# Performance work log

Measured on AMD Instinct MI355X. Metric: run time of the kernel, lower is better.

## Reference

```python
import jax, jax.numpy as jnp
import numpy as np

N_NODES = 100000
N_EDGES = 1600000
IN_C, HID_C, OUT_C = 128, 128, 64


def gcn_conv(x, src, dst, n_nodes, W, b):
    # PyG GCNConv (normalize=True, add_self_loops=True):
    # out = D^{-1/2} (A+I) D^{-1/2} (x @ W^T) + b
    h = x @ W.T                                   # [N, out]
    deg = jax.ops.segment_sum(jnp.ones(src.shape, x.dtype), dst,
                              num_segments=n_nodes)  # includes self-loops
    dinv = jnp.where(deg > 0, jax.lax.rsqrt(deg), 0.0)
    norm = dinv[src] * dinv[dst]                  # [E+N]
    msg = h[src] * norm[:, None]                  # gather + scale
    out = jax.ops.segment_sum(msg, dst, num_segments=n_nodes)
    return out + b


def setup_inputs() -> dict:
    key = jax.random.key(0)
    ks = jax.random.split(key, 8)
    x = jax.random.normal(ks[0], (N_NODES, IN_C), dtype=jnp.float32)
    edge_index = jax.random.randint(ks[1], (2, N_EDGES), 0, N_NODES, dtype=jnp.int64)

    def lin(k, fan_out, fan_in):
        s = 1.0 / np.sqrt(fan_in)
        kw, kb = jax.random.split(k)
        W = jax.random.uniform(kw, (fan_out, fan_in), jnp.float32, -s, s)
        b = jax.random.uniform(kb, (fan_out,), jnp.float32, -s, s)
        return W, b

    W1, b1 = lin(ks[2], HID_C, IN_C)
    W2, b2 = lin(ks[3], HID_C, HID_C)
    W3, b3 = lin(ks[4], OUT_C, HID_C)
    return {"x": x, "edge_index": edge_index,
            "W1": W1, "b1": b1, "W2": W2, "b2": b2, "W3": W3, "b3": b3}


def reference(x, edge_index, W1, b1, W2, b2, W3, b3):
    n = x.shape[0]
    loop = jnp.arange(n, dtype=edge_index.dtype)
    src = jnp.concatenate([edge_index[0], loop])  # add self-loops once; identical per layer
    dst = jnp.concatenate([edge_index[1], loop])
    h = gcn_conv(x, src, dst, n, W1, b1)
    h = jax.nn.relu(h)
    h = gcn_conv(h, src, dst, n, W2, b2)
    h = jax.nn.relu(h)
    h = gcn_conv(h, src, dst, n, W3, b3)
    return h
```

## Files before the change

### kernel.cpp

```cpp
#include <hip/hip_runtime.h>


#define NPB 256
#define CAP 4672
#define BIN_WGS 512

typedef short bfrag __attribute__((ext_vector_type(8)));
typedef float f32x4 __attribute__((ext_vector_type(4)));
typedef unsigned short u16x8 __attribute__((ext_vector_type(8)));

__global__ __launch_bounds__(256) void bin_edges(const int* __restrict__ src,
                                                 const int* __restrict__ dst,
                                                 int* __restrict__ cur,
                                                 int* __restrict__ binned,
                                                 int E, int B) {
  __shared__ int lc[512];
  __shared__ int lbase[512];
  const int t = threadIdx.x;
  const int chunk = (E + BIN_WGS - 1) / BIN_WGS;
  const int e0 = blockIdx.x * chunk;
  const int e1 = min(E, e0 + chunk);

  for (int i = t; i < B; i += 256) lc[i] = 0;
  __syncthreads();
  for (int e = e0 + t; e < e1; e += 256) {
    int d = dst[e];
    atomicAdd(&lc[d >> 8], 1);
  }
  __syncthreads();
  for (int i = t; i < B; i += 256) {
    int c = lc[i];
    lbase[i] = c ? atomicAdd(&cur[i], c) : 0;
    lc[i] = 0;
  }
  __syncthreads();
  for (int e = e0 + t; e < e1; e += 256) {
    int d = dst[e];
    int s = __builtin_nontemporal_load(&src[e]);
    int bk = d >> 8;
    int p = lbase[bk] + atomicAdd(&lc[bk], 1);
    if (p < (bk + 1) * CAP)
      binned[p] = ((d & 255) << 24) | s;
  }
}

__global__ __launch_bounds__(256) void build_buckets(const int* __restrict__ binned,
                                                     const int* __restrict__ cur,
                                                     int* __restrict__ cols,
                                                     int2* __restrict__ off2,
                                                     float* __restrict__ dinv,
                                                     int N) {
  __shared__ int eb[CAP];
  __shared__ int ob[CAP];
  __shared__ int lc[256];
  __shared__ int sc[256];
  const int b = blockIdx.x;
  const int t = threadIdx.x;
  const int base = b * CAP;
  const int cntb = min(cur[b] - base, CAP);

  for (int i = t; i < cntb; i += 256) eb[i] = binned[base + i];
  lc[t] = 0;
  __syncthreads();
  for (int i = t; i < cntb; i += 256)
    atomicAdd(&lc[(unsigned)eb[i] >> 24], 1);
  __syncthreads();
  int myc = lc[t];
  sc[t] = myc;
  __syncthreads();
  for (int d = 1; d < 256; d <<= 1) {
    int a = (t >= d) ? sc[t - d] : 0;
    __syncthreads();
    sc[t] += a;
    __syncthreads();
  }
  int excl = sc[t] - myc;
  int node = b * NPB + t;
  if (node < N) {
    off2[node] = make_int2(base + excl, base + excl + myc);
    dinv[node] = rsqrtf((float)(myc + 1));
  }
  lc[t] = excl;
  __syncthreads();
  for (int i = t; i < cntb; i += 256) {
    int e = eb[i];
    int p = atomicAdd(&lc[(unsigned)e >> 24], 1);
    ob[p] = e & 0xFFFFFF;
  }
  __syncthreads();
  for (int i = t; i < cntb; i += 256) cols[base + i] = ob[i];
}

__device__ inline unsigned short bf16rne(float x) {
  unsigned u = __float_as_uint(x);
  return (unsigned short)((u + 0x7FFFu + ((u >> 16) & 1u)) >> 16);
}
__device__ inline float bf16lo(unsigned q) { return __uint_as_float(q << 16); }
__device__ inline float bf16hi(unsigned q) { return __uint_as_float(q & 0xFFFF0000u); }

__global__ __launch_bounds__(256) void split_w3(const float* __restrict__ W1,
                                                const float* __restrict__ W2,
                                                const float* __restrict__ W3,
                                                unsigned short* __restrict__ w1h,
                                                unsigned short* __restrict__ w1l,
                                                unsigned short* __restrict__ w2h,
                                                unsigned short* __restrict__ w2l,
                                                unsigned short* __restrict__ w3h,
                                                unsigned short* __restrict__ w3l,
                                                int* __restrict__ cur, int B) {
  int i = blockIdx.x * 256 + threadIdx.x;
  const float* W;
  unsigned short *hi, *lo;
  int j;
  if (i < 16384) {
    W = W1; hi = w1h; lo = w1l; j = i;
  } else if (i < 32768) {
    W = W2; hi = w2h; lo = w2l; j = i - 16384;
  } else if (i < 40960) {
    W = W3; hi = w3h; lo = w3l; j = i - 32768;
  } else if (i < 40960 + B) {
    cur[i - 40960] = (i - 40960) * CAP;
    return;
  } else {
    return;
  }
  float v = W[j];
  unsigned short h = bf16rne(v);
  hi[j] = h;
  lo[j] = bf16rne(v - __uint_as_float((unsigned)h << 16));
}

#define LDP 136

template <int OUTC, bool CSOUT>
__global__ __launch_bounds__(256) void gemm_planes(const unsigned short* __restrict__ Xh,
                                                   const unsigned short* __restrict__ Xl,
                                                   const unsigned short* __restrict__ Whg,
                                                   const unsigned short* __restrict__ Wlg,
                                                   const float* __restrict__ dinv,
                                                   unsigned short* __restrict__ Y,
                                                   int M) {
  constexpr int CHUNKS = OUTC / 64;
  __shared__ unsigned short Whi[64 * LDP], Wlo[64 * LDP];
  const int tid = threadIdx.x;
  const int m_base = blockIdx.x * 64;
  const int lane = tid & 63;
  const int wv = tid >> 6;
  const int col_l = lane & 15;
  const int quad = lane >> 4;
  const size_t arow = (size_t)min(m_base + wv * 16 + col_l, M - 1) * 128;
  const int bBase = col_l * LDP + quad * 8;

  bfrag aH[4], aL[4];
#pragma unroll
  for (int ks = 0; ks < 4; ++ks) {
    aH[ks] = *(const bfrag*)(Xh + arow + ks * 32 + quad * 8);
    aL[ks] = *(const bfrag*)(Xl + arow + ks * 32 + quad * 8);
  }

  f32x4 acc[CHUNKS][4];
#pragma unroll
  for (int c2 = 0; c2 < CHUNKS; ++c2)
#pragma unroll
    for (int t = 0; t < 4; ++t) acc[c2][t] = {0.f, 0.f, 0.f, 0.f};

#pragma unroll
  for (int c2 = 0; c2 < CHUNKS; ++c2) {
    if (c2) __syncthreads();
    for (int idx = tid; idx < 64 * 16; idx += 256) {
      int r = idx >> 4, g = idx & 15;
      *(u16x8*)(Whi + r * LDP + g * 8) =
          *(const u16x8*)(Whg + (size_t)(c2 * 64 + r) * 128 + g * 8);
      *(u16x8*)(Wlo + r * LDP + g * 8) =
          *(const u16x8*)(Wlg + (size_t)(c2 * 64 + r) * 128 + g * 8);
    }
    __syncthreads();
#pragma unroll
    for (int ks = 0; ks < 4; ++ks) {
#pragma unroll
      for (int t = 0; t < 4; ++t) {
        int bo = bBase + t * 16 * LDP + ks * 32;
        bfrag bHi = *(const bfrag*)(Whi + bo);
        bfrag bLo = *(const bfrag*)(Wlo + bo);
        acc[c2][t] = __builtin_amdgcn_mfma_f32_16x16x32_bf16(aH[ks], bHi, acc[c2][t], 0, 0, 0);
        acc[c2][t] = __builtin_amdgcn_mfma_f32_16x16x32_bf16(aL[ks], bHi, acc[c2][t], 0, 0, 0);
        acc[c2][t] = __builtin_amdgcn_mfma_f32_16x16x32_bf16(aH[ks], bLo, acc[c2][t], 0, 0, 0);
      }
    }
  }

#pragma unroll
  for (int r = 0; r < 4; ++r) {
    int row = m_base + wv * 16 + quad * 4 + r;
    if (row < M) {
      float s = dinv[row];
#pragma unroll
      for (int c2 = 0; c2 < CHUNKS; ++c2)
#pragma unroll
        for (int t = 0; t < 4; ++t) {
          unsigned short h = bf16rne(acc[c2][t][r] * s);
          if (CSOUT)
            Y[((size_t)c2 * M + row) * 64 + t * 16 + col_l] = h;
          else
            Y[(size_t)row * OUTC + c2 * 64 + t * 16 + col_l] = h;
        }
    }
  }
}

template <int OUTC, bool CSOUT>
__global__ __launch_bounds__(256) void gemm_xsplit(const float* __restrict__ X,
                                                   const unsigned short* __restrict__ Whg,
                                                   const unsigned short* __restrict__ Wlg,
                                                   const float* __restrict__ dinv,
                                                   unsigned short* __restrict__ Y,
                                                   int M) {
  constexpr int CHUNKS = OUTC / 64;
  __shared__ unsigned short Whi[64 * LDP], Wlo[64 * LDP];
  const int tid = threadIdx.x;
  const int m_base = blockIdx.x * 64;
  const int lane = tid & 63;
  const int wv = tid >> 6;
  const int col_l = lane & 15;
  const int quad = lane >> 4;
  const size_t arow = (size_t)min(m_base + wv * 16 + col_l, M - 1) * 128;
  const int bBase = col_l * LDP + quad * 8;

  bfrag aH[4], aL[4];
#pragma unroll
  for (int ks = 0; ks < 4; ++ks) {
    float4 v0 = *(const float4*)(X + arow + ks * 32 + quad * 8);
    float4 v1 = *(const float4*)(X + arow + ks * 32 + quad * 8 + 4);
    float vv[8] = {v0.x, v0.y, v0.z, v0.w, v1.x, v1.y, v1.z, v1.w};
#pragma unroll
    for (int j = 0; j < 8; ++j) {
      unsigned short h = bf16rne(vv[j]);
      aH[ks][j] = (short)h;
      aL[ks][j] = (short)bf16rne(vv[j] - __uint_as_float((unsigned)h << 16));
    }
  }

  f32x4 acc[CHUNKS][4];
#pragma unroll
  for (int c2 = 0; c2 < CHUNKS; ++c2)
#pragma unroll
    for (int t = 0; t < 4; ++t) acc[c2][t] = {0.f, 0.f, 0.f, 0.f};

#pragma unroll
  for (int c2 = 0; c2 < CHUNKS; ++c2) {
    if (c2) __syncthreads();
    for (int idx = tid; idx < 64 * 16; idx += 256) {
      int r = idx >> 4, g = idx & 15;
      *(u16x8*)(Whi + r * LDP + g * 8) =
          *(const u16x8*)(Whg + (size_t)(c2 * 64 + r) * 128 + g * 8);
      *(u16x8*)(Wlo + r * LDP + g * 8) =
          *(const u16x8*)(Wlg + (size_t)(c2 * 64 + r) * 128 + g * 8);
    }
    __syncthreads();
#pragma unroll
    for (int ks = 0; ks < 4; ++ks) {
#pragma unroll
      for (int t = 0; t < 4; ++t) {
        int bo = bBase + t * 16 * LDP + ks * 32;
        bfrag bHi = *(const bfrag*)(Whi + bo);
        bfrag bLo = *(const bfrag*)(Wlo + bo);
        acc[c2][t] = __builtin_amdgcn_mfma_f32_16x16x32_bf16(aH[ks], bHi, acc[c2][t], 0, 0, 0);
        acc[c2][t] = __builtin_amdgcn_mfma_f32_16x16x32_bf16(aL[ks], bHi, acc[c2][t], 0, 0, 0);
        acc[c2][t] = __builtin_amdgcn_mfma_f32_16x16x32_bf16(aH[ks], bLo, acc[c2][t], 0, 0, 0);
      }
    }
  }

#pragma unroll
  for (int r = 0; r < 4; ++r) {
    int row = m_base + wv * 16 + quad * 4 + r;
    if (row < M) {
      float s = dinv[row];
#pragma unroll
      for (int c2 = 0; c2 < CHUNKS; ++c2)
#pragma unroll
        for (int t = 0; t < 4; ++t) {
          unsigned short h = bf16rne(acc[c2][t][r] * s);
          if (CSOUT)
            Y[((size_t)c2 * M + row) * 64 + t * 16 + col_l] = h;
          else
            Y[(size_t)row * OUTC + c2 * 64 + t * 16 + col_l] = h;
        }
    }
  }
}

__device__ inline void acc_add(float* a, uint4 d) {
  a[0] += bf16lo(d.x); a[1] += bf16hi(d.x);
  a[2] += bf16lo(d.y); a[3] += bf16hi(d.y);
  a[4] += bf16lo(d.z); a[5] += bf16hi(d.z);
  a[6] += bf16lo(d.w); a[7] += bf16hi(d.w);
}

__global__ __launch_bounds__(256) void aggregate_h2(const unsigned short* __restrict__ xs,
                                                    const int2* __restrict__ off2,
                                                    const int* __restrict__ cols,
                                                    const float* __restrict__ dinv,
                                                    const float* __restrict__ bias,
                                                    unsigned short* __restrict__ oh,
                                                    unsigned short* __restrict__ ol,
                                                    int N) {
  const int cg = blockIdx.x & 1;
  const int tile = blockIdx.x >> 1;
  const int t = threadIdx.x;
  const int gl = t & 7;
  const int node = tile * 32 + (t >> 3);
  if (node >= N) return;

  const char* xb = (const char*)xs + (size_t)cg * N * 128;
  const unsigned go = (unsigned)gl * 16;

  float acc[8];
  {
    uint4 d = *(const uint4*)(xb + (size_t)node * 128 + go);
    acc[0] = bf16lo(d.x); acc[1] = bf16hi(d.x);
    acc[2] = bf16lo(d.y); acc[3] = bf16hi(d.y);
    acc[4] = bf16lo(d.z); acc[5] = bf16hi(d.z);
    acc[6] = bf16lo(d.w); acc[7] = bf16hi(d.w);
  }

  const int2 oo = off2[node];
  const int en = oo.y;
  for (int e0 = oo.x; e0 < en; e0 += 8) {
    int col = __builtin_nontemporal_load(&cols[min(e0 + gl, en - 1)]);
    int m = en - e0;
    if (m > 8) m = 8;
    const int c1 = m - 1;
    for (int j = 0; j < m; j += 4) {
      int s0 = __shfl(col, min(j,     c1), 8);
      int s1 = __shfl(col, min(j + 1, c1), 8);
      int s2 = __shfl(col, min(j + 2, c1), 8);
      int s3 = __shfl(col, min(j + 3, c1), 8);
      uint4 d0 = *(const uint4*)(xb + (size_t)s0 * 128 + go);
      uint4 d1 = *(const uint4*)(xb + (size_t)s1 * 128 + go);
      uint4 d2 = *(const uint4*)(xb + (size_t)s2 * 128 + go);
      uint4 d3 = *(const uint4*)(xb + (size_t)s3 * 128 + go);
// ... 107 lines not shown
    f32x4 oB = {h[4], h[5], h[6], h[7]};
    __builtin_nontemporal_store(oA, (f32x4*)(outf + (size_t)node * C + gl * 8));
    __builtin_nontemporal_store(oB, (f32x4*)(outf + (size_t)node * C + gl * 8 + 4));
  }
}


extern "C" void kernel_launch(void* const* d_in, const int* in_sizes, int n_in,
                              void* d_out, int out_size, void* d_ws, size_t ws_size,
                              hipStream_t stream) {
  const float* x  = (const float*)d_in[0];
  const int*   ei = (const int*)d_in[1];
  const float* W1 = (const float*)d_in[2];
  const float* b1 = (const float*)d_in[3];
  const float* W2 = (const float*)d_in[4];
  const float* b2 = (const float*)d_in[5];
  const float* W3 = (const float*)d_in[6];
  const float* b3 = (const float*)d_in[7];

  const int N = in_sizes[0] / 128;
  const int E = in_sizes[1] / 2;
  const int* src = ei;
  const int* dst = ei + E;
  const int B = (N + NPB - 1) / NPB;

  char* w = (char*)d_ws;
  size_t p = 0;
  auto alloc = [&](size_t bytes) -> void* {
    void* r = w + p;
    p = (p + bytes + 255) & ~(size_t)255;
    return r;
  };
  float*    dinv   = (float*)alloc((size_t)N * 4);
  int2*     off2   = (int2*)alloc((size_t)N * 8);
  int*      cur    = (int*)alloc((size_t)B * 4);
  int*      binned = (int*)alloc((size_t)B * CAP * 4);
  int*      cols   = (int*)alloc((size_t)B * CAP * 4);
  unsigned short* xsb = (unsigned short*)alloc((size_t)N * 128 * 2);
  unsigned short* hh  = (unsigned short*)alloc((size_t)N * 128 * 2);
  unsigned short* hl  = (unsigned short*)alloc((size_t)N * 128 * 2);
  unsigned short* w1h = (unsigned short*)alloc(128 * 128 * 2);
  unsigned short* w1l = (unsigned short*)alloc(128 * 128 * 2);
  unsigned short* w2h = (unsigned short*)alloc(128 * 128 * 2);
  unsigned short* w2l = (unsigned short*)alloc(128 * 128 * 2);
  unsigned short* w3h = (unsigned short*)alloc(64 * 128 * 2);
  unsigned short* w3l = (unsigned short*)alloc(64 * 128 * 2);

  split_w3<<<(40960 + B + 255) / 256, 256, 0, stream>>>(W1, W2, W3, w1h, w1l,
                                                        w2h, w2l, w3h, w3l,
                                                        cur, B);
  bin_edges<<<BIN_WGS, 256, 0, stream>>>(src, dst, cur, binned, E, B);
  build_buckets<<<B, 256, 0, stream>>>(binned, cur, cols, off2, dinv, N);

  const int gb = (N + 63) / 64;
  const int ah2 = ((N + 31) / 32) * 2;
  const int ab64 = (N + 31) / 32;

  gemm_xsplit<128, true><<<gb, 256, 0, stream>>>(x, w1h, w1l, dinv, xsb, N);
  aggregate_h2<<<ah2, 256, 0, stream>>>(xsb, off2, cols, dinv, b1, hh, hl, N);
  gemm_planes<128, true><<<gb, 256, 0, stream>>>(hh, hl, w2h, w2l, dinv, xsb, N);
  aggregate_h2<<<ah2, 256, 0, stream>>>(xsb, off2, cols, dinv, b2, hh, hl, N);
  gemm_planes<64, false><<<gb, 256, 0, stream>>>(hh, hl, w3h, w3l, dinv, xsb, N);
  aggregate4<64, false, false><<<ab64, 256, 0, stream>>>(xsb, off2, cols, dinv, b3,
                                                         (float*)d_out, nullptr,
                                                         nullptr, N);
}
```

Baseline: 376.2 us.

## Double GEMM row tile to 128 and split aggregation launches into halves

```diff
diff --git a/kernel.cpp b/kernel.cpp
--- a/kernel.cpp
+++ b/kernel.cpp
@@ -143,26 +143,31 @@
   constexpr int CHUNKS = OUTC / 64;
   __shared__ unsigned short Whi[64 * LDP], Wlo[64 * LDP];
   const int tid = threadIdx.x;
-  const int m_base = blockIdx.x * 64;
+  const int m_base = blockIdx.x * 128;
   const int lane = tid & 63;
   const int wv = tid >> 6;
   const int col_l = lane & 15;
   const int quad = lane >> 4;
-  const size_t arow = (size_t)min(m_base + wv * 16 + col_l, M - 1) * 128;
   const int bBase = col_l * LDP + quad * 8;
 
-  bfrag aH[4], aL[4];
-#pragma unroll
-  for (int ks = 0; ks < 4; ++ks) {
-    aH[ks] = *(const bfrag*)(Xh + arow + ks * 32 + quad * 8);
-    aL[ks] = *(const bfrag*)(Xl + arow + ks * 32 + quad * 8);
-  }
-
-  f32x4 acc[CHUNKS][4];
-#pragma unroll
-  for (int c2 = 0; c2 < CHUNKS; ++c2)
-#pragma unroll
-    for (int t = 0; t < 4; ++t) acc[c2][t] = {0.f, 0.f, 0.f, 0.f};
+  bfrag aH[2][4], aL[2][4];
+#pragma unroll
+  for (int mt = 0; mt < 2; ++mt) {
+    const size_t arow = (size_t)min(m_base + mt * 64 + wv * 16 + col_l, M - 1) * 128;
+#pragma unroll
+    for (int ks = 0; ks < 4; ++ks) {
+      aH[mt][ks] = *(const bfrag*)(Xh + arow + ks * 32 + quad * 8);
+      aL[mt][ks] = *(const bfrag*)(Xl + arow + ks * 32 + quad * 8);
+    }
+  }
+
+  f32x4 acc[2][CHUNKS][4];
+#pragma unroll
+  for (int mt = 0; mt < 2; ++mt)
+#pragma unroll
+    for (int c2 = 0; c2 < CHUNKS; ++c2)
+#pragma unroll
+      for (int t = 0; t < 4; ++t) acc[mt][c2][t] = {0.f, 0.f, 0.f, 0.f};
 
 #pragma unroll
   for (int c2 = 0; c2 < CHUNKS; ++c2) {
@@ -182,30 +187,35 @@
         int bo = bBase + t * 16 * LDP + ks * 32;
         bfrag bHi = *(const bfrag*)(Whi + bo);
         bfrag bLo = *(const bfrag*)(Wlo + bo);
-        acc[c2][t] = __builtin_amdgcn_mfma_f32_16x16x32_bf16(aH[ks], bHi, acc[c2][t], 0, 0, 0);
-        acc[c2][t] = __builtin_amdgcn_mfma_f32_16x16x32_bf16(aL[ks], bHi, acc[c2][t], 0, 0, 0);
-        acc[c2][t] = __builtin_amdgcn_mfma_f32_16x16x32_bf16(aH[ks], bLo, acc[c2][t], 0, 0, 0);
+#pragma unroll
+        for (int mt = 0; mt < 2; ++mt) {
+          acc[mt][c2][t] = __builtin_amdgcn_mfma_f32_16x16x32_bf16(aH[mt][ks], bHi, acc[mt][c2][t], 0, 0, 0);
+          acc[mt][c2][t] = __builtin_amdgcn_mfma_f32_16x16x32_bf16(aL[mt][ks], bHi, acc[mt][c2][t], 0, 0, 0);
+          acc[mt][c2][t] = __builtin_amdgcn_mfma_f32_16x16x32_bf16(aH[mt][ks], bLo, acc[mt][c2][t], 0, 0, 0);
+        }
       }
     }
   }
 
 #pragma unroll
-  for (int r = 0; r < 4; ++r) {
-    int row = m_base + wv * 16 + quad * 4 + r;
-    if (row < M) {
-      float s = dinv[row];
-#pragma unroll
-      for (int c2 = 0; c2 < CHUNKS; ++c2)
-#pragma unroll
-        for (int t = 0; t < 4; ++t) {
-          unsigned short h = bf16rne(acc[c2][t][r] * s);
-          if (CSOUT)
-            Y[((size_t)c2 * M + row) * 64 + t * 16 + col_l] = h;
-          else
-            Y[(size_t)row * OUTC + c2 * 64 + t * 16 + col_l] = h;
-        }
-    }
-  }
+  for (int mt = 0; mt < 2; ++mt)
+#pragma unroll
+    for (int r = 0; r < 4; ++r) {
+      int row = m_base + mt * 64 + wv * 16 + quad * 4 + r;
+      if (row < M) {
+        float s = dinv[row];
+#pragma unroll
+        for (int c2 = 0; c2 < CHUNKS; ++c2)
+#pragma unroll
+          for (int t = 0; t < 4; ++t) {
+            unsigned short h = bf16rne(acc[mt][c2][t][r] * s);
+            if (CSOUT)
+              Y[((size_t)c2 * M + row) * 64 + t * 16 + col_l] = h;
+            else
+              Y[(size_t)row * OUTC + c2 * 64 + t * 16 + col_l] = h;
+          }
+      }
+    }
 }
 
 template <int OUTC, bool CSOUT>
@@ -218,33 +228,38 @@
   constexpr int CHUNKS = OUTC / 64;
   __shared__ unsigned short Whi[64 * LDP], Wlo[64 * LDP];
   const int tid = threadIdx.x;
-  const int m_base = blockIdx.x * 64;
+  const int m_base = blockIdx.x * 128;
   const int lane = tid & 63;
   const int wv = tid >> 6;
   const int col_l = lane & 15;
   const int quad = lane >> 4;
-  const size_t arow = (size_t)min(m_base + wv * 16 + col_l, M - 1) * 128;
   const int bBase = col_l * LDP + quad * 8;
 
-  bfrag aH[4], aL[4];
-#pragma unroll
-  for (int ks = 0; ks < 4; ++ks) {
-    float4 v0 = *(const float4*)(X + arow + ks * 32 + quad * 8);
-    float4 v1 = *(const float4*)(X + arow + ks * 32 + quad * 8 + 4);
-    float vv[8] = {v0.x, v0.y, v0.z, v0.w, v1.x, v1.y, v1.z, v1.w};
-#pragma unroll
-    for (int j = 0; j < 8; ++j) {
-      unsigned short h = bf16rne(vv[j]);
-      aH[ks][j] = (short)h;
-      aL[ks][j] = (short)bf16rne(vv[j] - __uint_as_float((unsigned)h << 16));
-    }
-  }
-
-  f32x4 acc[CHUNKS][4];
-#pragma unroll
-  for (int c2 = 0; c2 < CHUNKS; ++c2)
-#pragma unroll
-    for (int t = 0; t < 4; ++t) acc[c2][t] = {0.f, 0.f, 0.f, 0.f};
+  bfrag aH[2][4], aL[2][4];
+#pragma unroll
+  for (int mt = 0; mt < 2; ++mt) {
+    const size_t arow = (size_t)min(m_base + mt * 64 + wv * 16 + col_l, M - 1) * 128;
+#pragma unroll
+    for (int ks = 0; ks < 4; ++ks) {
+      float4 v0 = *(const float4*)(X + arow + ks * 32 + quad * 8);
+      float4 v1 = *(const float4*)(X + arow + ks * 32 + quad * 8 + 4);
+      float vv[8] = {v0.x, v0.y, v0.z, v0.w, v1.x, v1.y, v1.z, v1.w};
+#pragma unroll
+      for (int j = 0; j < 8; ++j) {
+        unsigned short h = bf16rne(vv[j]);
+        aH[mt][ks][j] = (short)h;
+        aL[mt][ks][j] = (short)bf16rne(vv[j] - __uint_as_float((unsigned)h << 16));
+      }
+    }
+  }
+
+  f32x4 acc[2][CHUNKS][4];
+#pragma unroll
+  for (int mt = 0; mt < 2; ++mt)
+#pragma unroll
+    for (int c2 = 0; c2 < CHUNKS; ++c2)
+#pragma unroll
+      for (int t = 0; t < 4; ++t) acc[mt][c2][t] = {0.f, 0.f, 0.f, 0.f};
 
 #pragma unroll
   for (int c2 = 0; c2 < CHUNKS; ++c2) {
@@ -264,30 +279,35 @@
         int bo = bBase + t * 16 * LDP + ks * 32;
         bfrag bHi = *(const bfrag*)(Whi + bo);
         bfrag bLo = *(const bfrag*)(Wlo + bo);
-        acc[c2][t] = __builtin_amdgcn_mfma_f32_16x16x32_bf16(aH[ks], bHi, acc[c2][t], 0, 0, 0);
-        acc[c2][t] = __builtin_amdgcn_mfma_f32_16x16x32_bf16(aL[ks], bHi, acc[c2][t], 0, 0, 0);
-        acc[c2][t] = __builtin_amdgcn_mfma_f32_16x16x32_bf16(aH[ks], bLo, acc[c2][t], 0, 0, 0);
+#pragma unroll
+        for (int mt = 0; mt < 2; ++mt) {
+          acc[mt][c2][t] = __builtin_amdgcn_mfma_f32_16x16x32_bf16(aH[mt][ks], bHi, acc[mt][c2][t], 0, 0, 0);
+          acc[mt][c2][t] = __builtin_amdgcn_mfma_f32_16x16x32_bf16(aL[mt][ks], bHi, acc[mt][c2][t], 0, 0, 0);
+          acc[mt][c2][t] = __builtin_amdgcn_mfma_f32_16x16x32_bf16(aH[mt][ks], bLo, acc[mt][c2][t], 0, 0, 0);
+        }
       }
     }
   }
 
 #pragma unroll
-  for (int r = 0; r < 4; ++r) {
-    int row = m_base + wv * 16 + quad * 4 + r;
-    if (row < M) {
-      float s = dinv[row];
-#pragma unroll
-      for (int c2 = 0; c2 < CHUNKS; ++c2)
-#pragma unroll
-        for (int t = 0; t < 4; ++t) {
-          unsigned short h = bf16rne(acc[c2][t][r] * s);
-          if (CSOUT)
-            Y[((size_t)c2 * M + row) * 64 + t * 16 + col_l] = h;
-          else
-            Y[(size_t)row * OUTC + c2 * 64 + t * 16 + col_l] = h;
-        }
-    }
-  }
+  for (int mt = 0; mt < 2; ++mt)
+#pragma unroll
+    for (int r = 0; r < 4; ++r) {
+      int row = m_base + mt * 64 + wv * 16 + quad * 4 + r;
+      if (row < M) {
+        float s = dinv[row];
+#pragma unroll
+        for (int c2 = 0; c2 < CHUNKS; ++c2)
+#pragma unroll
+          for (int t = 0; t < 4; ++t) {
+            unsigned short h = bf16rne(acc[mt][c2][t][r] * s);
+            if (CSOUT)
+              Y[((size_t)c2 * M + row) * 64 + t * 16 + col_l] = h;
+            else
+              Y[(size_t)row * OUTC + c2 * 64 + t * 16 + col_l] = h;
+          }
+      }
+    }
 }
 
 __device__ inline void acc_add(float* a, uint4 d) {
@@ -304,9 +324,9 @@
                                                     const float* __restrict__ bias,
                                                     unsigned short* __restrict__ oh,
                                                     unsigned short* __restrict__ ol,
-                                                    int N) {
+                                                    int tile0, int N) {
   const int cg = blockIdx.x & 1;
-  const int tile = blockIdx.x >> 1;
+  const int tile = tile0 + (blockIdx.x >> 1);
   const int t = threadIdx.x;
   const int gl = t & 7;
   const int node = tile * 32 + (t >> 3);
@@ -500,14 +520,17 @@
   bin_edges<<<BIN_WGS, 256, 0, stream>>>(src, dst, cur, binned, E, B);
   build_buckets<<<B, 256, 0, stream>>>(binned, cur, cols, off2, dinv, N);
 
-  const int gb = (N + 63) / 64;
-  const int ah2 = ((N + 31) / 32) * 2;
+  const int gb = (N + 127) / 128;
+  const int T = (N + 31) / 32;
+  const int TH = (T + 1) / 2;
   const int ab64 = (N + 31) / 32;
 
   gemm_xsplit<128, true><<<gb, 256, 0, stream>>>(x, w1h, w1l, dinv, xsb, N);
-  aggregate_h2<<<ah2, 256, 0, stream>>>(xsb, off2, cols, dinv, b1, hh, hl, N);
+  aggregate_h2<<<TH * 2, 256, 0, stream>>>(xsb, off2, cols, dinv, b1, hh, hl, 0, N);
+  aggregate_h2<<<(T - TH) * 2, 256, 0, stream>>>(xsb, off2, cols, dinv, b1, hh, hl, TH, N);
   gemm_planes<128, true><<<gb, 256, 0, stream>>>(hh, hl, w2h, w2l, dinv, xsb, N);
-  aggregate_h2<<<ah2, 256, 0, stream>>>(xsb, off2, cols, dinv, b2, hh, hl, N);
+  aggregate_h2<<<TH * 2, 256, 0, stream>>>(xsb, off2, cols, dinv, b2, hh, hl, 0, N);
+  aggregate_h2<<<(T - TH) * 2, 256, 0, stream>>>(xsb, off2, cols, dinv, b2, hh, hl, TH, N);
   gemm_planes<64, false><<<gb, 256, 0, stream>>>(hh, hl, w3h, w3l, dinv, xsb, N);
   aggregate4<64, false, false><<<ab64, 256, 0, stream>>>(xsb, off2, cols, dinv, b3,
                                                          (float*)d_out, nullptr,
```

After: 393.8 us. +4.7%, slower.

## Make GEMM kernels persistent with resident weights and prefetch of next row tile

Applied to the files above, without the earlier changes.

```diff
diff --git a/kernel.cpp b/kernel.cpp
--- a/kernel.cpp
+++ b/kernel.cpp
@@ -133,160 +133,194 @@
 #define LDP 136
 
 template <int OUTC, bool CSOUT>
-__global__ __launch_bounds__(256) void gemm_planes(const unsigned short* __restrict__ Xh,
-                                                   const unsigned short* __restrict__ Xl,
-                                                   const unsigned short* __restrict__ Whg,
-                                                   const unsigned short* __restrict__ Wlg,
-                                                   const float* __restrict__ dinv,
-                                                   unsigned short* __restrict__ Y,
-                                                   int M) {
-  constexpr int CHUNKS = OUTC / 64;
-  __shared__ unsigned short Whi[64 * LDP], Wlo[64 * LDP];
+__global__ __launch_bounds__(256) void gemm_planes_p(const unsigned short* __restrict__ Xh,
+                                                     const unsigned short* __restrict__ Xl,
+                                                     const unsigned short* __restrict__ Whg,
+                                                     const unsigned short* __restrict__ Wlg,
+                                                     const float* __restrict__ dinv,
+                                                     unsigned short* __restrict__ Y,
+                                                     int M, int ntiles) {
+  constexpr int CT = OUTC / 16;
+  __shared__ unsigned short Whi[OUTC * LDP], Wlo[OUTC * LDP];
   const int tid = threadIdx.x;
-  const int m_base = blockIdx.x * 64;
+
+  for (int idx = tid; idx < OUTC * 16; idx += 256) {
+    int r = idx >> 4, g = idx & 15;
+    *(u16x8*)(Whi + r * LDP + g * 8) = *(const u16x8*)(Whg + (size_t)r * 128 + g * 8);
+    *(u16x8*)(Wlo + r * LDP + g * 8) = *(const u16x8*)(Wlg + (size_t)r * 128 + g * 8);
+  }
+  __syncthreads();
+
   const int lane = tid & 63;
   const int wv = tid >> 6;
   const int col_l = lane & 15;
   const int quad = lane >> 4;
-  const size_t arow = (size_t)min(m_base + wv * 16 + col_l, M - 1) * 128;
   const int bBase = col_l * LDP + quad * 8;
-
-  bfrag aH[4], aL[4];
-#pragma unroll
-  for (int ks = 0; ks < 4; ++ks) {
-    aH[ks] = *(const bfrag*)(Xh + arow + ks * 32 + quad * 8);
-    aL[ks] = *(const bfrag*)(Xl + arow + ks * 32 + quad * 8);
-  }
-
-  f32x4 acc[CHUNKS][4];
-#pragma unroll
-  for (int c2 = 0; c2 < CHUNKS; ++c2)
-#pragma unroll
-    for (int t = 0; t < 4; ++t) acc[c2][t] = {0.f, 0.f, 0.f, 0.f};
-
-#pragma unroll
-  for (int c2 = 0; c2 < CHUNKS; ++c2) {
-    if (c2) __syncthreads();
-    for (int idx = tid; idx < 64 * 16; idx += 256) {
-      int r = idx >> 4, g = idx & 15;
-      *(u16x8*)(Whi + r * LDP + g * 8) =
-          *(const u16x8*)(Whg + (size_t)(c2 * 64 + r) * 128 + g * 8);
-      *(u16x8*)(Wlo + r * LDP + g * 8) =
-          *(const u16x8*)(Wlg + (size_t)(c2 * 64 + r) * 128 + g * 8);
-    }
-    __syncthreads();
+  const int G = gridDim.x;
+
+  int tt = blockIdx.x;
+  if (tt >= ntiles) return;
+
+  bfrag aH[4], aL[4], nH[4], nL[4];
+  {
+    const size_t arow = (size_t)min(tt * 64 + wv * 16 + col_l, M - 1) * 128;
 #pragma unroll
     for (int ks = 0; ks < 4; ++ks) {
-#pragma unroll
-      for (int t = 0; t < 4; ++t) {
-        int bo = bBase + t * 16 * LDP + ks * 32;
+      aH[ks] = *(const bfrag*)(Xh + arow + ks * 32 + quad * 8);
+      aL[ks] = *(const bfrag*)(Xl + arow + ks * 32 + quad * 8);
+    }
+  }
+
+  while (true) {
+    const int tn = tt + G;
+    const bool have_next = tn < ntiles;
+    if (have_next) {
+      const size_t arow = (size_t)min(tn * 64 + wv * 16 + col_l, M - 1) * 128;
+#pragma unroll
+      for (int ks = 0; ks < 4; ++ks) {
+        nH[ks] = *(const bfrag*)(Xh + arow + ks * 32 + quad * 8);
+        nL[ks] = *(const bfrag*)(Xl + arow + ks * 32 + quad * 8);
+      }
+    }
+
+    f32x4 acc[CT];
+#pragma unroll
+    for (int ct = 0; ct < CT; ++ct) acc[ct] = {0.f, 0.f, 0.f, 0.f};
+#pragma unroll
+    for (int ks = 0; ks < 4; ++ks) {
+#pragma unroll
+      for (int ct = 0; ct < CT; ++ct) {
+        int bo = bBase + ct * 16 * LDP + ks * 32;
         bfrag bHi = *(const bfrag*)(Whi + bo);
         bfrag bLo = *(const bfrag*)(Wlo + bo);
-        acc[c2][t] = __builtin_amdgcn_mfma_f32_16x16x32_bf16(aH[ks], bHi, acc[c2][t], 0, 0, 0);
-        acc[c2][t] = __builtin_amdgcn_mfma_f32_16x16x32_bf16(aL[ks], bHi, acc[c2][t], 0, 0, 0);
-        acc[c2][t] = __builtin_amdgcn_mfma_f32_16x16x32_bf16(aH[ks], bLo, acc[c2][t], 0, 0, 0);
-      }
-    }
-  }
-
-#pragma unroll
-  for (int r = 0; r < 4; ++r) {
-    int row = m_base + wv * 16 + quad * 4 + r;
-    if (row < M) {
-      float s = dinv[row];
-#pragma unroll
-      for (int c2 = 0; c2 < CHUNKS; ++c2)
-#pragma unroll
-        for (int t = 0; t < 4; ++t) {
-          unsigned short h = bf16rne(acc[c2][t][r] * s);
+        acc[ct] = __builtin_amdgcn_mfma_f32_16x16x32_bf16(aH[ks], bHi, acc[ct], 0, 0, 0);
+        acc[ct] = __builtin_amdgcn_mfma_f32_16x16x32_bf16(aL[ks], bHi, acc[ct], 0, 0, 0);
+        acc[ct] = __builtin_amdgcn_mfma_f32_16x16x32_bf16(aH[ks], bLo, acc[ct], 0, 0, 0);
+      }
+    }
+
+#pragma unroll
+    for (int r = 0; r < 4; ++r) {
+      int row = tt * 64 + wv * 16 + quad * 4 + r;
+      if (row < M) {
+        float s = dinv[row];
+#pragma unroll
+        for (int ct = 0; ct < CT; ++ct) {
+          unsigned short h = bf16rne(acc[ct][r] * s);
           if (CSOUT)
-            Y[((size_t)c2 * M + row) * 64 + t * 16 + col_l] = h;
+            Y[((size_t)(ct >> 2) * M + row) * 64 + (ct & 3) * 16 + col_l] = h;
           else
-            Y[(size_t)row * OUTC + c2 * 64 + t * 16 + col_l] = h;
+            Y[(size_t)row * OUTC + ct * 16 + col_l] = h;
         }
-    }
+      }
+    }
+
+    if (!have_next) break;
+#pragma unroll
+    for (int ks = 0; ks < 4; ++ks) { aH[ks] = nH[ks]; aL[ks] = nL[ks]; }
+    tt = tn;
   }
 }
 
 template <int OUTC, bool CSOUT>
-__global__ __launch_bounds__(256) void gemm_xsplit(const float* __restrict__ X,
-                                                   const unsigned short* __restrict__ Whg,
-                                                   const unsigned short* __restrict__ Wlg,
-                                                   const float* __restrict__ dinv,
-                                                   unsigned short* __restrict__ Y,
-                                                   int M) {
-  constexpr int CHUNKS = OUTC / 64;
-  __shared__ unsigned short Whi[64 * LDP], Wlo[64 * LDP];
+__global__ __launch_bounds__(256) void gemm_xsplit_p(const float* __restrict__ X,
+                                                     const unsigned short* __restrict__ Whg,
+                                                     const unsigned short* __restrict__ Wlg,
+                                                     const float* __restrict__ dinv,
+                                                     unsigned short* __restrict__ Y,
+                                                     int M, int ntiles) {
+  constexpr int CT = OUTC / 16;
+  __shared__ unsigned short Whi[OUTC * LDP], Wlo[OUTC * LDP];
   const int tid = threadIdx.x;
-  const int m_base = blockIdx.x * 64;
+
+  for (int idx = tid; idx < OUTC * 16; idx += 256) {
+    int r = idx >> 4, g = idx & 15;
+    *(u16x8*)(Whi + r * LDP + g * 8) = *(const u16x8*)(Whg + (size_t)r * 128 + g * 8);
+    *(u16x8*)(Wlo + r * LDP + g * 8) = *(const u16x8*)(Wlg + (size_t)r * 128 + g * 8);
+  }
+  __syncthreads();
+
   const int lane = tid & 63;
   const int wv = tid >> 6;
   const int col_l = lane & 15;
   const int quad = lane >> 4;
-  const size_t arow = (size_t)min(m_base + wv * 16 + col_l, M - 1) * 128;
   const int bBase = col_l * LDP + quad * 8;
-
-  bfrag aH[4], aL[4];
-#pragma unroll
-  for (int ks = 0; ks < 4; ++ks) {
-    float4 v0 = *(const float4*)(X + arow + ks * 32 + quad * 8);
-    float4 v1 = *(const float4*)(X + arow + ks * 32 + quad * 8 + 4);
-    float vv[8] = {v0.x, v0.y, v0.z, v0.w, v1.x, v1.y, v1.z, v1.w};
-#pragma unroll
-    for (int j = 0; j < 8; ++j) {
-      unsigned short h = bf16rne(vv[j]);
-      aH[ks][j] = (short)h;
-      aL[ks][j] = (short)bf16rne(vv[j] - __uint_as_float((unsigned)h << 16));
-    }
-  }
-
-  f32x4 acc[CHUNKS][4];
-#pragma unroll
-  for (int c2 = 0; c2 < CHUNKS; ++c2)
-#pragma unroll
-    for (int t = 0; t < 4; ++t) acc[c2][t] = {0.f, 0.f, 0.f, 0.f};
-
-#pragma unroll
-  for (int c2 = 0; c2 < CHUNKS; ++c2) {
-    if (c2) __syncthreads();
-    for (int idx = tid; idx < 64 * 16; idx += 256) {
-      int r = idx >> 4, g = idx & 15;
-      *(u16x8*)(Whi + r * LDP + g * 8) =
-          *(const u16x8*)(Whg + (size_t)(c2 * 64 + r) * 128 + g * 8);
-      *(u16x8*)(Wlo + r * LDP + g * 8) =
-          *(const u16x8*)(Wlg + (size_t)(c2 * 64 + r) * 128 + g * 8);
-    }
-    __syncthreads();
+  const int G = gridDim.x;
+
+  int tt = blockIdx.x;
+  if (tt >= ntiles) return;
+
+  float4 r0[4], r1[4], n0[4], n1[4];
+  {
+    const size_t arow = (size_t)min(tt * 64 + wv * 16 + col_l, M - 1) * 128;
 #pragma unroll
     for (int ks = 0; ks < 4; ++ks) {
-#pragma unroll
-      for (int t = 0; t < 4; ++t) {
-        int bo = bBase + t * 16 * LDP + ks * 32;
+      r0[ks] = *(const float4*)(X + arow + ks * 32 + quad * 8);
+      r1[ks] = *(const float4*)(X + arow + ks * 32 + quad * 8 + 4);
+    }
+  }
+
+  while (true) {
+    const int tn = tt + G;
+    const bool have_next = tn < ntiles;
+    if (have_next) {
+      const size_t arow = (size_t)min(tn * 64 + wv * 16 + col_l, M - 1) * 128;
+#pragma unroll
+      for (int ks = 0; ks < 4; ++ks) {
+        n0[ks] = *(const float4*)(X + arow + ks * 32 + quad * 8);
+        n1[ks] = *(const float4*)(X + arow + ks * 32 + quad * 8 + 4);
+      }
+    }
+
+    bfrag aH[4], aL[4];
+#pragma unroll
+    for (int ks = 0; ks < 4; ++ks) {
+      float vv[8] = {r0[ks].x, r0[ks].y, r0[ks].z, r0[ks].w,
+                     r1[ks].x, r1[ks].y, r1[ks].z, r1[ks].w};
+#pragma unroll
+      for (int j = 0; j < 8; ++j) {
+        unsigned short h = bf16rne(vv[j]);
+        aH[ks][j] = (short)h;
+        aL[ks][j] = (short)bf16rne(vv[j] - __uint_as_float((unsigned)h << 16));
+      }
+    }
+
+    f32x4 acc[CT];
+#pragma unroll
+    for (int ct = 0; ct < CT; ++ct) acc[ct] = {0.f, 0.f, 0.f, 0.f};
+#pragma unroll
+    for (int ks = 0; ks < 4; ++ks) {
+#pragma unroll
+      for (int ct = 0; ct < CT; ++ct) {
+        int bo = bBase + ct * 16 * LDP + ks * 32;
         bfrag bHi = *(const bfrag*)(Whi + bo);
         bfrag bLo = *(const bfrag*)(Wlo + bo);
-        acc[c2][t] = __builtin_amdgcn_mfma_f32_16x16x32_bf16(aH[ks], bHi, acc[c2][t], 0, 0, 0);
-        acc[c2][t] = __builtin_amdgcn_mfma_f32_16x16x32_bf16(aL[ks], bHi, acc[c2][t], 0, 0, 0);
-        acc[c2][t] = __builtin_amdgcn_mfma_f32_16x16x32_bf16(aH[ks], bLo, acc[c2][t], 0, 0, 0);
-      }
-    }
-  }
-
-#pragma unroll
-  for (int r = 0; r < 4; ++r) {
-    int row = m_base + wv * 16 + quad * 4 + r;
-    if (row < M) {
-      float s = dinv[row];
-#pragma unroll
-      for (int c2 = 0; c2 < CHUNKS; ++c2)
-#pragma unroll
-        for (int t = 0; t < 4; ++t) {
-          unsigned short h = bf16rne(acc[c2][t][r] * s);
+        acc[ct] = __builtin_amdgcn_mfma_f32_16x16x32_bf16(aH[ks], bHi, acc[ct], 0, 0, 0);
+        acc[ct] = __builtin_amdgcn_mfma_f32_16x16x32_bf16(aL[ks], bHi, acc[ct], 0, 0, 0);
+        acc[ct] = __builtin_amdgcn_mfma_f32_16x16x32_bf16(aH[ks], bLo, acc[ct], 0, 0, 0);
+      }
+    }
+
+#pragma unroll
+    for (int r = 0; r < 4; ++r) {
+      int row = tt * 64 + wv * 16 + quad * 4 + r;
+      if (row < M) {
+        float s = dinv[row];
+#pragma unroll
+        for (int ct = 0; ct < CT; ++ct) {
+          unsigned short h = bf16rne(acc[ct][r] * s);
           if (CSOUT)
-            Y[((size_t)c2 * M + row) * 64 + t * 16 + col_l] = h;
+            Y[((size_t)(ct >> 2) * M + row) * 64 + (ct & 3) * 16 + col_l] = h;
           else
-            Y[(size_t)row * OUTC + c2 * 64 + t * 16 + col_l] = h;
+            Y[(size_t)row * OUTC + ct * 16 + col_l] = h;
         }
-    }
+      }
+    }
+
+    if (!have_next) break;
+#pragma unroll
+    for (int ks = 0; ks < 4; ++ks) { r0[ks] = n0[ks]; r1[ks] = n1[ks]; }
+    tt = tn;
   }
 }
 
@@ -500,15 +534,17 @@
   bin_edges<<<BIN_WGS, 256, 0, stream>>>(src, dst, cur, binned, E, B);
   build_buckets<<<B, 256, 0, stream>>>(binned, cur, cols, off2, dinv, N);
 
-  const int gb = (N + 63) / 64;
-  const int ah2 = ((N + 31) / 32) * 2;
+  const int ntiles = (N + 63) / 64;
+  const int G128 = 512;
+  const int G64  = 1024;
+  const int T = (N + 31) / 32;
   const int ab64 = (N + 31) / 32;
 
-  gemm_xsplit<128, true><<<gb, 256, 0, stream>>>(x, w1h, w1l, dinv, xsb, N);
-  aggregate_h2<<<ah2, 256, 0, stream>>>(xsb, off2, cols, dinv, b1, hh, hl, N);
-  gemm_planes<128, true><<<gb, 256, 0, stream>>>(hh, hl, w2h, w2l, dinv, xsb, N);
-  aggregate_h2<<<ah2, 256, 0, stream>>>(xsb, off2, cols, dinv, b2, hh, hl, N);
-  gemm_planes<64, false><<<gb, 256, 0, stream>>>(hh, hl, w3h, w3l, dinv, xsb, N);
+  gemm_xsplit_p<128, true><<<G128, 256, 0, stream>>>(x, w1h, w1l, dinv, xsb, N, ntiles);
+  aggregate_h2<<<T * 2, 256, 0, stream>>>(xsb, off2, cols, dinv, b1, hh, hl, N);
+  gemm_planes_p<128, true><<<G128, 256, 0, stream>>>(hh, hl, w2h, w2l, dinv, xsb, N, ntiles);
+  aggregate_h2<<<T * 2, 256, 0, stream>>>(xsb, off2, cols, dinv, b2, hh, hl, N);
+  gemm_planes_p<64, false><<<G64, 256, 0, stream>>>(hh, hl, w3h, w3l, dinv, xsb, N, ntiles);
   aggregate4<64, false, false><<<ab64, 256, 0, stream>>>(xsb, off2, cols, dinv, b3,
                                                          (float*)d_out, nullptr,
                                                          nullptr, N);
```

Result: no change. 382.9 us (+1.8%).

## Compute degrees via atomics early and overlap edge binning with first GEMM

Applied to the files above, without the earlier changes.

```diff
diff --git a/kernel.cpp b/kernel.cpp
--- a/kernel.cpp
+++ b/kernel.cpp
@@ -4,93 +4,12 @@
 #define NPB 256
 #define CAP 4672
 #define BIN_WGS 512
+#define LDP 136
 
 typedef short bfrag __attribute__((ext_vector_type(8)));
 typedef float f32x4 __attribute__((ext_vector_type(4)));
 typedef unsigned short u16x8 __attribute__((ext_vector_type(8)));
 
-__global__ __launch_bounds__(256) void bin_edges(const int* __restrict__ src,
-                                                 const int* __restrict__ dst,
-                                                 int* __restrict__ cur,
-                                                 int* __restrict__ binned,
-                                                 int E, int B) {
-  __shared__ int lc[512];
-  __shared__ int lbase[512];
-  const int t = threadIdx.x;
-  const int chunk = (E + BIN_WGS - 1) / BIN_WGS;
-  const int e0 = blockIdx.x * chunk;
-  const int e1 = min(E, e0 + chunk);
-
-  for (int i = t; i < B; i += 256) lc[i] = 0;
-  __syncthreads();
-  for (int e = e0 + t; e < e1; e += 256) {
-    int d = dst[e];
-    atomicAdd(&lc[d >> 8], 1);
-  }
-  __syncthreads();
-  for (int i = t; i < B; i += 256) {
-    int c = lc[i];
-    lbase[i] = c ? atomicAdd(&cur[i], c) : 0;
-    lc[i] = 0;
-  }
-  __syncthreads();
-  for (int e = e0 + t; e < e1; e += 256) {
-    int d = dst[e];
-    int s = __builtin_nontemporal_load(&src[e]);
-    int bk = d >> 8;
-    int p = lbase[bk] + atomicAdd(&lc[bk], 1);
-    if (p < (bk + 1) * CAP)
-      binned[p] = ((d & 255) << 24) | s;
-  }
-}
-
-__global__ __launch_bounds__(256) void build_buckets(const int* __restrict__ binned,
-                                                     const int* __restrict__ cur,
-                                                     int* __restrict__ cols,
-                                                     int2* __restrict__ off2,
-                                                     float* __restrict__ dinv,
-                                                     int N) {
-  __shared__ int eb[CAP];
-  __shared__ int ob[CAP];
-  __shared__ int lc[256];
-  __shared__ int sc[256];
-  const int b = blockIdx.x;
-  const int t = threadIdx.x;
-  const int base = b * CAP;
-  const int cntb = min(cur[b] - base, CAP);
-
-  for (int i = t; i < cntb; i += 256) eb[i] = binned[base + i];
-  lc[t] = 0;
-  __syncthreads();
-  for (int i = t; i < cntb; i += 256)
-    atomicAdd(&lc[(unsigned)eb[i] >> 24], 1);
-  __syncthreads();
-  int myc = lc[t];
-  sc[t] = myc;
-  __syncthreads();
-  for (int d = 1; d < 256; d <<= 1) {
-    int a = (t >= d) ? sc[t - d] : 0;
-    __syncthreads();
-    sc[t] += a;
-    __syncthreads();
-  }
-  int excl = sc[t] - myc;
-  int node = b * NPB + t;
-  if (node < N) {
-    off2[node] = make_int2(base + excl, base + excl + myc);
-    dinv[node] = rsqrtf((float)(myc + 1));
-  }
-  lc[t] = excl;
-  __syncthreads();
-  for (int i = t; i < cntb; i += 256) {
-    int e = eb[i];
-    int p = atomicAdd(&lc[(unsigned)e >> 24], 1);
-    ob[p] = e & 0xFFFFFF;
-  }
-  __syncthreads();
-  for (int i = t; i < cntb; i += 256) cols[base + i] = ob[i];
-}
-
 __device__ inline unsigned short bf16rne(float x) {
   unsigned u = __float_as_uint(x);
   return (unsigned short)((u + 0x7FFFu + ((u >> 16) & 1u)) >> 16);
@@ -98,17 +17,31 @@
 __device__ inline float bf16lo(unsigned q) { return __uint_as_float(q << 16); }
 __device__ inline float bf16hi(unsigned q) { return __uint_as_float(q & 0xFFFF0000u); }
 
-__global__ __launch_bounds__(256) void split_w3(const float* __restrict__ W1,
-                                                const float* __restrict__ W2,
-                                                const float* __restrict__ W3,
-                                                unsigned short* __restrict__ w1h,
-                                                unsigned short* __restrict__ w1l,
-                                                unsigned short* __restrict__ w2h,
-                                                unsigned short* __restrict__ w2l,
-                                                unsigned short* __restrict__ w3h,
-                                                unsigned short* __restrict__ w3l,
-                                                int* __restrict__ cur, int B) {
-  int i = blockIdx.x * 256 + threadIdx.x;
+__global__ __launch_bounds__(256) void split_w3_deg(const float* __restrict__ W1,
+                                                    const float* __restrict__ W2,
+                                                    const float* __restrict__ W3,
+                                                    unsigned short* __restrict__ w1h,
+                                                    unsigned short* __restrict__ w1l,
+                                                    unsigned short* __restrict__ w2h,
+                                                    unsigned short* __restrict__ w2l,
+                                                    unsigned short* __restrict__ w3h,
+                                                    unsigned short* __restrict__ w3l,
+                                                    int* __restrict__ cur,
+                                                    int* __restrict__ deg,
+                                                    const int* __restrict__ dst,
+                                                    int B, int E, int NS) {
+  const int bid = blockIdx.x;
+  const int t = threadIdx.x;
+  if (bid >= NS) {
+    const int hb = bid - NS;
+    const int chunk = (E + BIN_WGS - 1) / BIN_WGS;
+    const int e0 = hb * chunk;
+    const int e1 = min(E, e0 + chunk);
+    for (int e = e0 + t; e < e1; e += 256)
+      atomicAdd(&deg[__builtin_nontemporal_load(&dst[e])], 1);
+    return;
+  }
+  int i = bid * 256 + t;
   const float* W;
   unsigned short *hi, *lo;
   int j;
@@ -130,7 +63,206 @@
   lo[j] = bf16rne(v - __uint_as_float((unsigned)h << 16));
 }
 
-#define LDP 136
+__global__ __launch_bounds__(256) void dinv_k(const int* __restrict__ deg,
+                                              float* __restrict__ dinv, int N) {
+  int i = blockIdx.x * 256 + threadIdx.x;
+  if (i < N) dinv[i] = rsqrtf((float)(deg[i] + 1));
+}
+
+__device__ inline void bin_edges_body(char* smem,
+                                      const int* __restrict__ src,
+                                      const int* __restrict__ dst,
+                                      int* __restrict__ cur,
+                                      int* __restrict__ binned,
+                                      int E, int B) {
+  int* lc = (int*)smem;
+  int* lbase = lc + 512;
+  const int t = threadIdx.x;
+  const int chunk = (E + BIN_WGS - 1) / BIN_WGS;
+  const int e0 = blockIdx.x * chunk;
+  const int e1 = min(E, e0 + chunk);
+
+  for (int i = t; i < B; i += 256) lc[i] = 0;
+  __syncthreads();
+  for (int e = e0 + t; e < e1; e += 256) {
+    int d = dst[e];
+    atomicAdd(&lc[d >> 8], 1);
+  }
+  __syncthreads();
+  for (int i = t; i < B; i += 256) {
+    int c = lc[i];
+    lbase[i] = c ? atomicAdd(&cur[i], c) : 0;
+    lc[i] = 0;
+  }
+  __syncthreads();
+  for (int e = e0 + t; e < e1; e += 256) {
+    int d = dst[e];
+    int s = __builtin_nontemporal_load(&src[e]);
+    int bk = d >> 8;
+    int p = lbase[bk] + atomicAdd(&lc[bk], 1);
+    if (p < (bk + 1) * CAP)
+      binned[p] = ((d & 255) << 24) | s;
+  }
+}
+
+__device__ inline void build_buckets_body(char* smem, int b,
+                                          const int* __restrict__ binned,
+                                          const int* __restrict__ cur,
+                                          int* __restrict__ cols,
+                                          int2* __restrict__ off2,
+                                          int N) {
+  int* eb = (int*)smem;
+  int* ob = eb + CAP;
+  int* lc = ob + CAP;
+  int* sc = lc + 256;
+  const int t = threadIdx.x;
+  const int base = b * CAP;
+  const int cntb = min(cur[b] - base, CAP);
+
+  for (int i = t; i < cntb; i += 256) eb[i] = binned[base + i];
+  lc[t] = 0;
+  __syncthreads();
+  for (int i = t; i < cntb; i += 256)
+    atomicAdd(&lc[(unsigned)eb[i] >> 24], 1);
+  __syncthreads();
+  int myc = lc[t];
+  sc[t] = myc;
+  __syncthreads();
+  for (int d = 1; d < 256; d <<= 1) {
+    int a = (t >= d) ? sc[t - d] : 0;
+    __syncthreads();
+    sc[t] += a;
+    __syncthreads();
+  }
+  int excl = sc[t] - myc;
+  int node = b * NPB + t;
+  if (node < N)
+    off2[node] = make_int2(base + excl, base + excl + myc);
+  lc[t] = excl;
+  __syncthreads();
+  for (int i = t; i < cntb; i += 256) {
+    int e = eb[i];
+    int p = atomicAdd(&lc[(unsigned)e >> 24], 1);
+    ob[p] = e & 0xFFFFFF;
+  }
+  __syncthreads();
+  for (int i = t; i < cntb; i += 256) cols[base + i] = ob[i];
+}
+
+__device__ inline void gemm_xsplit_body(char* smem, int mtile,
+                                        const float* __restrict__ X,
+                                        const unsigned short* __restrict__ Whg,
+                                        const unsigned short* __restrict__ Wlg,
+                                        const float* __restrict__ dinv,
+                                        unsigned short* __restrict__ Y,
+                                        int M) {
+  unsigned short* Whi = (unsigned short*)smem;
+  unsigned short* Wlo = Whi + 64 * LDP;
+  const int tid = threadIdx.x;
+  const int m_base = mtile * 64;
+  const int lane = tid & 63;
+  const int wv = tid >> 6;
+  const int col_l = lane & 15;
+  const int quad = lane >> 4;
+  const size_t arow = (size_t)min(m_base + wv * 16 + col_l, M - 1) * 128;
+  const int bBase = col_l * LDP + quad * 8;
+
+  bfrag aH[4], aL[4];
+#pragma unroll
+  for (int ks = 0; ks < 4; ++ks) {
+    float4 v0 = *(const float4*)(X + arow + ks * 32 + quad * 8);
+    float4 v1 = *(const float4*)(X + arow + ks * 32 + quad * 8 + 4);
+    float vv[8] = {v0.x, v0.y, v0.z, v0.w, v1.x, v1.y, v1.z, v1.w};
+#pragma unroll
+    for (int j = 0; j < 8; ++j) {
+      unsigned short h = bf16rne(vv[j]);
+      aH[ks][j] = (short)h;
+      aL[ks][j] = (short)bf16rne(vv[j] - __uint_as_float((unsigned)h << 16));
+    }
+  }
+
+  f32x4 acc[2][4];
+#pragma unroll
+  for (int c2 = 0; c2 < 2; ++c2)
+#pragma unroll
+    for (int t = 0; t < 4; ++t) acc[c2][t] = {0.f, 0.f, 0.f, 0.f};
+
+#pragma unroll
+  for (int c2 = 0; c2 < 2; ++c2) {
+    if (c2) __syncthreads();
+    for (int idx = tid; idx < 64 * 16; idx += 256) {
+      int r = idx >> 4, g = idx & 15;
+      *(u16x8*)(Whi + r * LDP + g * 8) =
+          *(const u16x8*)(Whg + (size_t)(c2 * 64 + r) * 128 + g * 8);
+      *(u16x8*)(Wlo + r * LDP + g * 8) =
+          *(const u16x8*)(Wlg + (size_t)(c2 * 64 + r) * 128 + g * 8);
+    }
+    __syncthreads();
+#pragma unroll
+    for (int ks = 0; ks < 4; ++ks) {
+#pragma unroll
+      for (int t = 0; t < 4; ++t) {
+        int bo = bBase + t * 16 * LDP + ks * 32;
+        bfrag bHi = *(const bfrag*)(Whi + bo);
+        bfrag bLo = *(const bfrag*)(Wlo + bo);
+        acc[c2][t] = __builtin_amdgcn_mfma_f32_16x16x32_bf16(aH[ks], bHi, acc[c2][t], 0, 0, 0);
+        acc[c2][t] = __builtin_amdgcn_mfma_f32_16x16x32_bf16(aL[ks], bHi, acc[c2][t], 0, 0, 0);
+        acc[c2][t] = __builtin_amdgcn_mfma_f32_16x16x32_bf16(aH[ks], bLo, acc[c2][t], 0, 0, 0);
+      }
+    }
+  }
+
+#pragma unroll
+  for (int r = 0; r < 4; ++r) {
+    int row = m_base + wv * 16 + quad * 4 + r;
+    if (row < M) {
+      float s = dinv[row];
+#pragma unroll
+      for (int c2 = 0; c2 < 2; ++c2)
+#pragma unroll
+        for (int t = 0; t < 4; ++t) {
+          unsigned short h = bf16rne(acc[c2][t][r] * s);
+          Y[((size_t)c2 * M + row) * 64 + t * 16 + col_l] = h;
+        }
+    }
+  }
+}
+
+__global__ __launch_bounds__(256) void fused_bin_gemm(const int* __restrict__ src,
+                                                      const int* __restrict__ dst,
+                                                      int* __restrict__ cur,
+                                                      int* __restrict__ binned,
+                                                      int E, int B,
+                                                      const float* __restrict__ X,
+                                                      const unsigned short* __restrict__ Whg,
+                                                      const unsigned short* __restrict__ Wlg,
+                                                      const float* __restrict__ dinv,
+                                                      unsigned short* __restrict__ Y,
+                                                      int M) {
+  __shared__ __align__(16) char smem[34816];
+  if (blockIdx.x < BIN_WGS)
+    bin_edges_body(smem, src, dst, cur, binned, E, B);
+  else
+    gemm_xsplit_body(smem, blockIdx.x - BIN_WGS, X, Whg, Wlg, dinv, Y, M);
+}
+
+__global__ __launch_bounds__(256) void fused_bb_gemm(const int* __restrict__ binned,
+                                                     const int* __restrict__ cur,
+                                                     int* __restrict__ cols,
+                                                     int2* __restrict__ off2,
+                                                     int N, int B,
+                                                     const float* __restrict__ X,
+                                                     const unsigned short* __restrict__ Whg,
+                                                     const unsigned short* __restrict__ Wlg,
+                                                     const float* __restrict__ dinv,
+                                                     unsigned short* __restrict__ Y,
+                                                     int T1) {
+  __shared__ __align__(16) char smem[39424];
+  if ((int)blockIdx.x < B)
+    build_buckets_body(smem, blockIdx.x, binned, cur, cols, off2, N);
+  else
+    gemm_xsplit_body(smem, T1 + blockIdx.x - B, X, Whg, Wlg, dinv, Y, N);
+}
 
 template <int OUTC, bool CSOUT>
 __global__ __launch_bounds__(256) void gemm_planes(const unsigned short* __restrict__ Xh,
@@ -156,88 +288,6 @@
   for (int ks = 0; ks < 4; ++ks) {
     aH[ks] = *(const bfrag*)(Xh + arow + ks * 32 + quad * 8);
     aL[ks] = *(const bfrag*)(Xl + arow + ks * 32 + quad * 8);
-  }
-
-  f32x4 acc[CHUNKS][4];
-#pragma unroll
-  for (int c2 = 0; c2 < CHUNKS; ++c2)
-#pragma unroll
-    for (int t = 0; t < 4; ++t) acc[c2][t] = {0.f, 0.f, 0.f, 0.f};
-
-#pragma unroll
-  for (int c2 = 0; c2 < CHUNKS; ++c2) {
-    if (c2) __syncthreads();
-    for (int idx = tid; idx < 64 * 16; idx += 256) {
-      int r = idx >> 4, g = idx & 15;
-      *(u16x8*)(Whi + r * LDP + g * 8) =
-          *(const u16x8*)(Whg + (size_t)(c2 * 64 + r) * 128 + g * 8);
-      *(u16x8*)(Wlo + r * LDP + g * 8) =
-          *(const u16x8*)(Wlg + (size_t)(c2 * 64 + r) * 128 + g * 8);
-    }
-    __syncthreads();
-#pragma unroll
-    for (int ks = 0; ks < 4; ++ks) {
-#pragma unroll
-      for (int t = 0; t < 4; ++t) {
-        int bo = bBase + t * 16 * LDP + ks * 32;
-        bfrag bHi = *(const bfrag*)(Whi + bo);
-        bfrag bLo = *(const bfrag*)(Wlo + bo);
-        acc[c2][t] = __builtin_amdgcn_mfma_f32_16x16x32_bf16(aH[ks], bHi, acc[c2][t], 0, 0, 0);
-        acc[c2][t] = __builtin_amdgcn_mfma_f32_16x16x32_bf16(aL[ks], bHi, acc[c2][t], 0, 0, 0);
-        acc[c2][t] = __builtin_amdgcn_mfma_f32_16x16x32_bf16(aH[ks], bLo, acc[c2][t], 0, 0, 0);
-      }
-    }
-  }
-
-#pragma unroll
-  for (int r = 0; r < 4; ++r) {
-    int row = m_base + wv * 16 + quad * 4 + r;
-    if (row < M) {
-      float s = dinv[row];
-#pragma unroll
-      for (int c2 = 0; c2 < CHUNKS; ++c2)
-#pragma unroll
-        for (int t = 0; t < 4; ++t) {
-          unsigned short h = bf16rne(acc[c2][t][r] * s);
-          if (CSOUT)
-            Y[((size_t)c2 * M + row) * 64 + t * 16 + col_l] = h;
-          else
-            Y[(size_t)row * OUTC + c2 * 64 + t * 16 + col_l] = h;
-        }
-    }
-  }
-}
-
-template <int OUTC, bool CSOUT>
-__global__ __launch_bounds__(256) void gemm_xsplit(const float* __restrict__ X,
-                                                   const unsigned short* __restrict__ Whg,
-                                                   const unsigned short* __restrict__ Wlg,
-                                                   const float* __restrict__ dinv,
-                                                   unsigned short* __restrict__ Y,
-                                                   int M) {
-  constexpr int CHUNKS = OUTC / 64;
-  __shared__ unsigned short Whi[64 * LDP], Wlo[64 * LDP];
-  const int tid = threadIdx.x;
-  const int m_base = blockIdx.x * 64;
-  const int lane = tid & 63;
-  const int wv = tid >> 6;
-  const int col_l = lane & 15;
-  const int quad = lane >> 4;
-  const size_t arow = (size_t)min(m_base + wv * 16 + col_l, M - 1) * 128;
-  const int bBase = col_l * LDP + quad * 8;
-
-  bfrag aH[4], aL[4];
-#pragma unroll
-  for (int ks = 0; ks < 4; ++ks) {
-    float4 v0 = *(const float4*)(X + arow + ks * 32 + quad * 8);
-    float4 v1 = *(const float4*)(X + arow + ks * 32 + quad * 8 + 4);
-    float vv[8] = {v0.x, v0.y, v0.z, v0.w, v1.x, v1.y, v1.z, v1.w};
-#pragma unroll
-    for (int j = 0; j < 8; ++j) {
-      unsigned short h = bf16rne(vv[j]);
-      aH[ks][j] = (short)h;
-      aL[ks][j] = (short)bf16rne(vv[j] - __uint_as_float((unsigned)h << 16));
-    }
   }
 
   f32x4 acc[CHUNKS][4];
@@ -480,6 +530,7 @@
     return r;
   };
   float*    dinv   = (float*)alloc((size_t)N * 4);
+  int*      deg    = (int*)alloc((size_t)N * 4);
   int2*     off2   = (int2*)alloc((size_t)N * 8);
   int*      cur    = (int*)alloc((size_t)B * 4);
   int*      binned = (int*)alloc((size_t)B * CAP * 4);
@@ -494,20 +545,27 @@
   unsigned short* w3h = (unsigned short*)alloc(64 * 128 * 2);
   unsigned short* w3l = (unsigned short*)alloc(64 * 128 * 2);
 
-  split_w3<<<(40960 + B + 255) / 256, 256, 0, stream>>>(W1, W2, W3, w1h, w1l,
-                                                        w2h, w2l, w3h, w3l,
-                                                        cur, B);
-  bin_edges<<<BIN_WGS, 256, 0, stream>>>(src, dst, cur, binned, E, B);
-  build_buckets<<<B, 256, 0, stream>>>(binned, cur, cols, off2, dinv, N);
-
+  const int NS = (40960 + B + 255) / 256;
+  const int ntiles = (N + 63) / 64;
+  const int T1 = min(600, ntiles);
   const int gb = (N + 63) / 64;
-  const int ah2 = ((N + 31) / 32) * 2;
+  const int T = (N + 31) / 32;
   const int ab64 = (N + 31) / 32;
 
-  gemm_xsplit<128, true><<<gb, 256, 0, stream>>>(x, w1h, w1l, dinv, xsb, N);
-  aggregate_h2<<<ah2, 256, 0, stream>>>(xsb, off2, cols, dinv, b1, hh, hl, N);
+  hipMemsetAsync(deg, 0, (size_t)N * 4, stream);
+  split_w3_deg<<<NS + BIN_WGS, 256, 0, stream>>>(W1, W2, W3, w1h, w1l, w2h, w2l,
+                                                 w3h, w3l, cur, deg, dst, B, E, NS);
+  dinv_k<<<(N + 255) / 256, 256, 0, stream>>>(deg, dinv, N);
+
+  fused_bin_gemm<<<BIN_WGS + T1, 256, 0, stream>>>(src, dst, cur, binned, E, B,
+                                                   x, w1h, w1l, dinv, xsb, N);
+  fused_bb_gemm<<<B + (ntiles - T1), 256, 0, stream>>>(binned, cur, cols, off2,
+                                                       N, B, x, w1h, w1l, dinv,
+                                                       xsb, T1);
+
+  aggregate_h2<<<T * 2, 256, 0, stream>>>(xsb, off2, cols, dinv, b1, hh, hl, N);
   gemm_planes<128, true><<<gb, 256, 0, stream>>>(hh, hl, w2h, w2l, dinv, xsb, N);
-  aggregate_h2<<<ah2, 256, 0, stream>>>(xsb, off2, cols, dinv, b2, hh, hl, N);
+  aggregate_h2<<<T * 2, 256, 0, stream>>>(xsb, off2, cols, dinv, b2, hh, hl, N);
   gemm_planes<64, false><<<gb, 256, 0, stream>>>(hh, hl, w3h, w3l, dinv, xsb, N);
   aggregate4<64, false, false><<<ab64, 256, 0, stream>>>(xsb, off2, cols, dinv, b3,
                                                          (float*)d_out, nullptr,
```

Measured after the change: 444.7 us. 1.18x slower.
